# Optimization experiments

Measured on AMD Instinct MI355X. Metric: run time of the kernel, lower is better.

The kernel has to match this reference:

```python
import jax, jax.numpy as jnp
import numpy as np

N, Y, D, B, K, CHUNK = 1024, 2, 128, 256, 16, 64
SCALE = 0.25      # slope of the soft partial order sigmoid
GAMMA = 0.05      # slope of the irrelevance sigmoid
TAU = 2.0 * D     # squared-distance threshold for irrelevance


def setup_inputs() -> dict:
    key = jax.random.key(0)
    ks = jax.random.split(key, 6)
    return {
        "X_train": jax.random.normal(ks[0], (N, D), jnp.float32),
        "X_default": jax.random.normal(ks[1], (Y, D), jnp.float32),
        "X_query": jax.random.normal(ks[2], (B, D), jnp.float32),
        "w_order": jax.random.normal(ks[3], (D,), jnp.float32) / np.float32(np.sqrt(D)),
        "w_base": jax.random.normal(ks[4], (D,), jnp.float32) / np.float32(np.sqrt(D)),
        "y_train_labels": jax.random.randint(ks[5], (N,), 0, Y, jnp.int32),
        "y_default_labels": jnp.arange(Y, dtype=jnp.int32),
    }


def _blocked_product(Wm, Es):
    """result[i,j] = prod_k (1 - Wm[i,k] * Es[k,j]), chunked over k (CHUNK)."""
    T = Wm.shape[0]
    pad = (-T) % CHUNK
    Wp = jnp.pad(Wm, ((0, 0), (0, pad)))   # zero pad -> factor (1-0)=1
    Ep = jnp.pad(Es, ((0, pad), (0, 0)))
    nch = Wp.shape[1] // CHUNK
    Wc = jnp.transpose(Wp.reshape(T, nch, CHUNK), (1, 0, 2))  # [nch, T, CHUNK]
    Ec = Ep.reshape(nch, CHUNK, T)                             # [nch, CHUNK, T]

    def body(carry, wk_ek):
        Wk, Ek = wk_ek  # [T, CHUNK], [CHUNK, T]
        term = jnp.prod(1.0 - Wk[:, :, None] * Ek[None, :, :], axis=1)  # [T, T]
        return carry * term, None

    res, _ = jax.lax.scan(jax.checkpoint(body), jnp.ones((T, T), Wm.dtype), (Wc, Ec))
    return res


def _fit_A(X, yf, w_order, n_default):
    """Build the (negated-attack) edge-weight matrix A of the casebase QBAF."""
    T = X.shape[0]
    is_default = jnp.arange(T) >= (T - n_default)  # default rows cannot attack
    # soft partial order: E[i,j] = sigma(SCALE * (p_i - p_j))  (attacker i vs target j)
    p = X @ w_order                                  # [T]
    E = jax.nn.sigmoid(SCALE * (p[:, None] - p[None, :]))
    Es = E * (1.0 - E.T)                             # strict ordering
    Es = jnp.where(is_default[:, None], 0.0, Es)     # defaults_not_attack
    same = (yf @ yf.T) > 0.5                         # same-label mask (one-hot)
    attacks = jnp.where(same, 0.0, Es)               # potential attacks: differing labels
    # minimal-attack blockers: same-label intermediates k with i<k<j block i->j
    Wm = jnp.where(same, Es, 0.0) * (1.0 - jnp.eye(T, dtype=Es.dtype))
    blocked = _blocked_product(Wm, Es)               # [T, T]
    # symmetric attacks between equal cases with differing labels
    sym = E * E.T
    sym = jnp.where(same, 0.0, sym)
    sym = jnp.where(is_default[:, None], 0.0, sym)
    return -(attacks * blocked + sym)


def reference(X_train, X_default, X_query, w_order, w_base, y_train_labels, y_default_labels):
    X = jnp.concatenate([X_train, X_default], axis=0)          # [T, D]
    yf = jnp.concatenate([
        jax.nn.one_hot(y_train_labels, Y, dtype=X.dtype),
        jax.nn.one_hot(y_default_labels, Y, dtype=X.dtype),
    ], axis=0)                                                 # [T, Y]
    A = _fit_A(X, yf, w_order, Y)                              # [T, T]
    base_logit = X @ w_base                                    # [T]
    # irrelevance edges: new case attacks irrelevant casebase arguments
    sq = (jnp.sum(X_query ** 2, 1)[:, None] + jnp.sum(X ** 2, 1)[None, :]
          - 2.0 * (X_query @ X.T))                             # [B, T]
    r = jax.nn.sigmoid(GAMMA * (sq - TAU))                     # [B, T]
    # gradual semantics: s <- sigma(logit(base) + sum_m A[m,n] s_m - r_n)
    s0 = jnp.broadcast_to(jax.nn.sigmoid(base_logit), (X_query.shape[0], X.shape[0]))
    def step(s, _):
        return jax.nn.sigmoid(base_logit[None, :] + s @ A - r), None
    s, _ = jax.lax.scan(step, s0, None, length=K)
    return s[:, -Y:]  # strengths of the default arguments -> [B, Y]
```

## Files before the change

kernel.cpp:

```cpp
#include <hip/hip_runtime.h>

#define NTRAIN 1024
#define NY 2
#define DDIM 128
#define NB 256
#define NITER 16
#define TT 1026
#define TP 1088
#define CP 640
#define TPP (2*CP)
#define SCALE_C 0.25f
#define GAMMA_C 0.05f
#define TAU_C 256.0f
#define IKCH 128

typedef _Float16 __attribute__((ext_vector_type(8))) f16x8;
typedef __attribute__((ext_vector_type(4))) float f32x4;
typedef __attribute__((ext_vector_type(8))) unsigned short us8;

union FR16 { ushort4 u[2]; f16x8 v; };

__device__ __forceinline__ float sigm(float x) {
    return 1.0f / (1.0f + __expf(-x));
}
__device__ __forceinline__ ushort f2u16(_Float16 h) {
    union { _Float16 h; ushort u; } x; x.h = h; return x.u;
}

__global__ void k_prep(const float* __restrict__ Xtr, const float* __restrict__ Xdef,
                       const float* __restrict__ worder, const float* __restrict__ wbase,
                       float* __restrict__ p, float* __restrict__ bl,
                       float* __restrict__ xsq) {
    int t = blockIdx.x;
    int tx = threadIdx.x;
    __shared__ float sp[128], sb[128], ss[128];
    float po = 0.f, bo = 0.f, sq = 0.f;
    if (t < TT) {
        const float* row = (t < NTRAIN) ? (Xtr + (size_t)t * DDIM)
                                        : (Xdef + (size_t)(t - NTRAIN) * DDIM);
        float x = row[tx];
        po = x * worder[tx];
        bo = x * wbase[tx];
        sq = x * x;
    }
    sp[tx] = po; sb[tx] = bo; ss[tx] = sq;
    __syncthreads();
    for (int off = 64; off > 0; off >>= 1) {
        if (tx < off) { sp[tx] += sp[tx+off]; sb[tx] += sb[tx+off]; ss[tx] += ss[tx+off]; }
        __syncthreads();
    }
    if (tx == 0) { p[t] = sp[0]; bl[t] = sb[0]; xsq[t] = ss[0]; }
}

__global__ void k_perm2(const int* __restrict__ ytr, const float* __restrict__ p,
                        int* __restrict__ map, float* __restrict__ pp) {
    __shared__ int cnt1[16];
    int tid = threadIdx.x;
    int w = tid >> 6, lane = tid & 63;
    for (int a = tid; a < TPP; a += 1024) map[a] = -1;
    int y = ytr[tid];
    unsigned long long b1 = __ballot(y == 1);
    if (lane == 0) cnt1[w] = (int)__popcll(b1);
    __syncthreads();
    int pref1 = 0;
    #pragma unroll
    for (int ww = 0; ww < 16; ww++) pref1 += (ww < w) ? cnt1[ww] : 0;
    int pref0 = w * 64 - pref1;
    unsigned long long mlt = ((unsigned long long)1 << lane) - 1ull;
    int rank = y ? (pref1 + (int)__popcll(b1 & mlt))
                 : (pref0 + (int)__popcll((~b1) & mlt));
    if (rank < CP - 1) map[y * CP + rank] = tid;
    if (tid < NY) map[tid * CP + CP - 1] = NTRAIN + tid;
    __syncthreads();
    for (int a = tid; a < TPP; a += 1024) {
        int m = map[a];
        pp[a] = (m >= 0) ? p[m] : 0.f;
    }
}

__global__ void k_es2(const int* __restrict__ map, const float* __restrict__ pp,
                      float* __restrict__ Es) {
    int b = blockIdx.x * 256 + threadIdx.x;
    int a = blockIdx.y;
    float v = 0.f;
    int mi = map[a], mj = map[b];
    if (mi >= 0 && mi < NTRAIN && mj >= 0) {
        float e = sigm(SCALE_C * (pp[a] - pp[b]));
        v = e * e;
    }
    Es[(size_t)a * TPP + b] = v;
}

#define KC 16
__global__ __launch_bounds__(256) void k_pblk2(const float* __restrict__ Es,
                                               float* __restrict__ P, int kspan) {
    __shared__ float Wt[KC][64 + 4];
    __shared__ float Et[KC][64 + 4];
    int c  = blockIdx.z & 1;
    int kz = blockIdx.z >> 1;
    int i0 = c * CP + blockIdx.y * 64;
    int j0 = (1 - c) * CP + blockIdx.x * 64;
    int ks = c * CP + kz * kspan, ke = ks + kspan;
    int tid = threadIdx.x;
    int tx = tid & 15, ty = tid >> 4;
    float prod[4][4];
    #pragma unroll
    for (int a = 0; a < 4; a++)
        #pragma unroll
        for (int b = 0; b < 4; b++) prod[a][b] = 1.f;

    for (int k0 = ks; k0 < ke; k0 += KC) {
        __syncthreads();
        #pragma unroll
        for (int e = tid; e < KC * 64; e += 256) {
            int kk = e & 15, ii = e >> 4;
            int gi = i0 + ii, gk = k0 + kk;
            float w = Es[(size_t)gi * TPP + gk];
            if (gi == gk) w = 0.f;
            Wt[kk][ii] = w;
        }
        #pragma unroll
        for (int e = tid; e < KC * 64; e += 256) {
            int jj = e & 63, kk = e >> 6;
            Et[kk][jj] = Es[(size_t)(k0 + kk) * TPP + j0 + jj];
        }
        __syncthreads();
        #pragma unroll
        for (int kk = 0; kk < KC; kk++) {
            float4 wv = *(const float4*)&Wt[kk][ty * 4];
            float4 ev = *(const float4*)&Et[kk][tx * 4];
            float w[4] = {wv.x, wv.y, wv.z, wv.w};
            float e[4] = {ev.x, ev.y, ev.z, ev.w};
            #pragma unroll
            for (int a = 0; a < 4; a++)
                #pragma unroll
                for (int b = 0; b < 4; b++)
                    prod[a][b] *= fmaf(-w[a], e[b], 1.f);
        }
    }
    float* Pz = P + (size_t)blockIdx.z * CP * CP;
    int jjl = blockIdx.x * 64 + tx * 4;
    #pragma unroll
    for (int a = 0; a < 4; a++) {
        int iil = blockIdx.y * 64 + ty * 4 + a;
        *(float4*)&Pz[(size_t)iil * CP + jjl] =
            make_float4(prod[a][0], prod[a][1], prod[a][2], prod[a][3]);
    }
}

__global__ __launch_bounds__(256) void k_afin2T(const float* __restrict__ P, int psplit,
                                                const int* __restrict__ map,
                                                const float* __restrict__ pp,
                                                const float* __restrict__ Es,
                                                ushort* __restrict__ ATF) {
    __shared__ float t[64][65];
    int n0 = blockIdx.y * 64;
    int d = (n0 >= CP) ? 1 : 0;
    int c = 1 - d;
    int kl0 = blockIdx.x * 64;
    int tid = threadIdx.x;
    for (int e = tid; e < 64 * 64; e += 256) {
        int r = e >> 6, col = e & 63;
        int iil = kl0 + r;
        int jjl = n0 - d * CP + col;
        size_t rem = (size_t)iil * CP + jjl;
        float prod = P[(size_t)c * CP * CP + rem];
        for (int kz = 1; kz < psplit; kz++)
            prod *= P[(size_t)(kz * 2 + c) * CP * CP + rem];
        int a = c * CP + iil, b = n0 + col;
        float v = 0.f;
        int mi = map[a], mj = map[b];
        if (mi >= 0 && mj >= 0) {
            float es = Es[(size_t)a * TPP + b];
            float x = SCALE_C * (pp[a] - pp[b]);
            float E = sigm(x);
            float sym = (mi < NTRAIN) ? E * (1.f - E) : 0.f;
            v = -(es * prod + sym);
        }
        t[r][col] = v;
    }
    __syncthreads();
    for (int e = tid; e < 64 * 64; e += 256) {
        int kk = e & 63, nn = e >> 6;
        ATF[(size_t)(n0 + nn) * CP + kl0 + kk] = f2u16((_Float16)t[kk][nn]);
    }
}

__global__ void k_cq2(const float* __restrict__ Xtr, const float* __restrict__ Xdef,
                      const float* __restrict__ Xq, const float* __restrict__ bl,
                      const int* __restrict__ map,
                      float* __restrict__ CT, ushort* __restrict__ SF) {
    int bq = blockIdx.y;
    int t = blockIdx.x * 256 + threadIdx.x;
    int mi = map[t];
    float cv = 0.f, sv = 0.f;
    if (mi >= 0) {
        const float4* q4 = (const float4*)(Xq + (size_t)bq * DDIM);
        const float* row = (mi < NTRAIN) ? (Xtr + (size_t)mi * DDIM)
                                         : (Xdef + (size_t)(mi - NTRAIN) * DDIM);
        const float4* x4 = (const float4*)row;
        float dot = 0.f, qs = 0.f, xs = 0.f;
        #pragma unroll
        for (int d = 0; d < DDIM / 4; d++) {
            float4 q = q4[d], x = x4[d];
            dot = fmaf(q.x, x.x, fmaf(q.y, x.y, fmaf(q.z, x.z, fmaf(q.w, x.w, dot))));
            qs  = fmaf(q.x, q.x, fmaf(q.y, q.y, fmaf(q.z, q.z, fmaf(q.w, q.w, qs))));
            xs  = fmaf(x.x, x.x, fmaf(x.y, x.y, fmaf(x.z, x.z, fmaf(x.w, x.w, xs))));
        }
        float sq = qs + xs - 2.f * dot;
        float r = sigm(GAMMA_C * (sq - TAU_C));
        cv = bl[mi] - r;
        sv = sigm(bl[mi]);
    }
    size_t o = (size_t)bq * TPP + t;
    CT[o] = cv;
    SF[o] = f2u16((_Float16)sv);
}

__device__ __forceinline__ float Aval(int m, int k) { return (float)((3*m + 7*k) % 13 - 6); }
__device__ __forceinline__ float Bval(int k, int n) { return (float)((5*k + 11*n) % 9 - 4); }

__global__ void k_probe(int* __restrict__ flag) {
    int lane = threadIdx.x;
    int lg = lane >> 4, li = lane & 15;
    FR16 fa, fb;
    #pragma unroll
    for (int j = 0; j < 8; j++) {
        int k = (j < 4) ? (4*lg + j) : (16 + 4*lg + (j - 4));
        fa.v[j] = (_Float16)Aval(li, k);
        fb.v[j] = (_Float16)Bval(k, li);
    }
    f32x4 acc = {0.f, 0.f, 0.f, 0.f};
    acc = __builtin_amdgcn_mfma_f32_16x16x32_f16(fa.v, fb.v, acc, 0, 0, 0);
    int ok = 1;
    #pragma unroll
    for (int r = 0; r < 4; r++) {
        int row = 4*lg + r, col = li;
        float ref = 0.f;
        for (int k = 0; k < 32; k++) ref += Aval(row, k) * Bval(k, col);
        if (acc[r] != ref) ok = 0;
    }
    int allok = __all(ok);
    if (lane == 0) *flag = allok ? 0 : 1;
}

__global__ __launch_bounds__(256) void k_ifp16(const ushort* __restrict__ SF,
                                               const ushort* __restrict__ ATF,
                                               const float* __restrict__ CT,
                                               const int* __restrict__ map,
                                               const int* __restrict__ flag,
                                               ushort* __restrict__ NF,
                                               float* __restrict__ out, int last) {
    __shared__ ushort SfL[32][IKCH + 8];
    __shared__ ushort AfL[32][IKCH + 8];
    int tid = threadIdx.x;
    int n0 = blockIdx.x * 32;
    int m0 = blockIdx.y * 32;
    int kb = (n0 >= CP) ? 0 : CP;
    int wv = tid >> 6, lane = tid & 63;
    int wm = wv >> 1, wn = wv & 1;
    int lg = lane >> 4, li = lane & 15;
    int hyp = *flag;
    int o0 = hyp ? (8*lg)     : (4*lg);
    int o1 = hyp ? (8*lg + 4) : (16 + 4*lg);
    int srow = tid >> 3, sc = tid & 7;

    const ushort* sfg = SF + (size_t)(m0 + srow) * TPP + kb;
    const ushort* afg = ATF + (size_t)(n0 + srow) * CP;

    f32x4 c0 = {0.f,0.f,0.f,0.f};

    us8 buf[4];
    #define ISSUE(dst, k0)                                            \
        dst[0] = *(const us8*)(sfg + (k0) + sc * 8);                  \
        dst[1] = *(const us8*)(sfg + (k0) + (sc + 8) * 8);            \
        dst[2] = *(const us8*)(afg + (k0) + sc * 8);                  \
        dst[3] = *(const us8*)(afg + (k0) + (sc + 8) * 8);

    ISSUE(buf, 0)

    #pragma unroll
    for (int ci = 0; ci < CP / IKCH; ci++) {
        __syncthreads();
        *(us8*)&SfL[srow][sc * 8]       = buf[0];
        *(us8*)&SfL[srow][(sc + 8) * 8] = buf[1];
        *(us8*)&AfL[srow][sc * 8]       = buf[2];
        *(us8*)&AfL[srow][(sc + 8) * 8] = buf[3];
        __syncthreads();
        us8 nbuf[4];
        if (ci + 1 < CP / IKCH) { ISSUE(nbuf, (ci + 1) * IKCH) }
        #pragma unroll
        for (int ks = 0; ks < IKCH / 32; ks++) {
            int ka = ks * 32;
            FR16 fs, fa;
            fs.u[0] = *(const ushort4*)&SfL[wm * 16 + li][ka + o0];
            fs.u[1] = *(const ushort4*)&SfL[wm * 16 + li][ka + o1];
            fa.u[0] = *(const ushort4*)&AfL[wn * 16 + li][ka + o0];
            fa.u[1] = *(const ushort4*)&AfL[wn * 16 + li][ka + o1];
            c0 = __builtin_amdgcn_mfma_f32_16x16x32_f16(fs.v, fa.v, c0, 0, 0, 0);
        }
        if (ci + 1 < CP / IKCH) {
            #pragma unroll
            for (int q = 0; q < 4; q++) buf[q] = nbuf[q];
        }
    }
    #undef ISSUE

    int col = n0 + wn * 16 + li;
    int valid = (map[col] >= 0);
    #pragma unroll
    for (int r = 0; r < 4; r++) {
        int row = m0 + wm * 16 + 4 * lg + r;
        float v = 0.f;
        if (valid) v = sigm(CT[(size_t)row * TPP + col] + c0[r]);
        NF[(size_t)row * TPP + col] = f2u16((_Float16)v);
        if (last && (col == CP - 1 || col == TPP - 1)) {
            int cc = (col == CP - 1) ? 0 : 1;
            out[row * NY + cc] = v;
        }
    }
}

extern "C" void kernel_launch(void* const* d_in, const int* in_sizes, int n_in,
                              void* d_out, int out_size, void* d_ws, size_t ws_size,
                              hipStream_t stream) {
    const float* Xtr    = (const float*)d_in[0];
    const float* Xdef   = (const float*)d_in[1];
    const float* Xq     = (const float*)d_in[2];
    const float* worder = (const float*)d_in[3];
    const float* wbase  = (const float*)d_in[4];
    const int*   ytr    = (const int*)d_in[5];

    const size_t MATP = (size_t)TPP * TPP * 4;
    const size_t VECP = (size_t)NB * TPP * 4;
    const size_t ATB2 = (size_t)TPP * CP * 2;
    const size_t SB   = (size_t)NB * TPP * 2;
    auto need = [&](int ps) {
        return (size_t)(8 * 8192) + MATP + (size_t)ps * 2 * CP * CP * 4
             + ATB2 + VECP + 2 * SB + 65536;
    };
    int psplit = 8;
    if (ws_size < need(8)) psplit = 4;
    if (ws_size < need(4)) psplit = 2;
    if (ws_size < need(2)) psplit = 1;
    int kspan = CP / psplit;

    char* ws = (char*)d_ws;
    size_t off = 0;
    auto alloc = [&](size_t bytes) {
        void* r = ws + off;
        off += (bytes + 255) & ~(size_t)255;
        return r;
    };
    float*  p    = (float*)alloc((size_t)TP * 4);
    float*  bl   = (float*)alloc((size_t)TP * 4);
    float*  xsq  = (float*)alloc((size_t)TP * 4);
    int*    map  = (int*)  alloc((size_t)TPP * 4);
    float*  pp   = (float*)alloc((size_t)TPP * 4);
    int*    flag = (int*)  alloc(256);
    float*  Es   = (float*)alloc(MATP);
    float*  P    = (float*)alloc((size_t)psplit * 2 * CP * CP * 4);
    ushort* ATF  = (ushort*)alloc(ATB2);
    float*  CT   = (float*)alloc(VECP);
    ushort* SF0  = (ushort*)alloc(SB);
    ushort* SF1  = (ushort*)alloc(SB);

    k_prep<<<TP, 128, 0, stream>>>(Xtr, Xdef, worder, wbase, p, bl, xsq);
    k_perm2<<<1, 1024, 0, stream>>>(ytr, p, map, pp);
    k_es2<<<dim3(TPP / 256, TPP), 256, 0, stream>>>(map, pp, Es);
    k_pblk2<<<dim3(CP / 64, CP / 64, 2 * psplit), 256, 0, stream>>>(Es, P, kspan);
    k_afin2T<<<dim3(CP / 64, TPP / 64), 256, 0, stream>>>(P, psplit, map, pp, Es, ATF);
    k_cq2<<<dim3(TPP / 256, NB), 256, 0, stream>>>(Xtr, Xdef, Xq, bl, map, CT, SF0);
    k_probe<<<1, 64, 0, stream>>>(flag);

    ushort *cf = SF0, *nf = SF1;
    for (int it = 0; it < NITER; it++) {
        k_ifp16<<<dim3(TPP / 32, NB / 32), 256, 0, stream>>>(cf, ATF, CT, map, flag, nf,
                                                             (float*)d_out,
                                                             it == NITER - 1 ? 1 : 0);
        ushort* t = cf; cf = nf; nf = t;
    }
}
```

Measured before the change: 288.5 us.

## Compute Es on the fly, batch query distances, and load full-K tiles in iteration kernel

Drops the materialised 1280x1280 Es matrix. The product kernel now recomputes sigmoid entries from the permuted p values and per-class counts, and the final A kernel recomputes E directly. The query-distance kernel handles 8 queries per block from shared memory and precomputes query norms separately. The iteration kernel loads the whole K=640 strip into LDS at once, uses 64-wide N tiles with two MFMA accumulators, and sets launch bounds to one block. This trades Es memory traffic for extra sigmoid work and larger LDS use, which may lower occupancy.

```diff
diff --git a/kernel.cpp b/kernel.cpp
--- a/kernel.cpp
+++ b/kernel.cpp
@@ -12,7 +12,6 @@
 #define SCALE_C 0.25f
 #define GAMMA_C 0.05f
 #define TAU_C 256.0f
-#define IKCH 128
 
 typedef _Float16 __attribute__((ext_vector_type(8))) f16x8;
 typedef __attribute__((ext_vector_type(4))) float f32x4;
@@ -29,31 +28,29 @@
 
 __global__ void k_prep(const float* __restrict__ Xtr, const float* __restrict__ Xdef,
                        const float* __restrict__ worder, const float* __restrict__ wbase,
-                       float* __restrict__ p, float* __restrict__ bl,
-                       float* __restrict__ xsq) {
+                       float* __restrict__ p, float* __restrict__ bl) {
     int t = blockIdx.x;
     int tx = threadIdx.x;
-    __shared__ float sp[128], sb[128], ss[128];
-    float po = 0.f, bo = 0.f, sq = 0.f;
+    __shared__ float sp[128], sb[128];
+    float po = 0.f, bo = 0.f;
     if (t < TT) {
         const float* row = (t < NTRAIN) ? (Xtr + (size_t)t * DDIM)
                                         : (Xdef + (size_t)(t - NTRAIN) * DDIM);
         float x = row[tx];
         po = x * worder[tx];
         bo = x * wbase[tx];
-        sq = x * x;
-    }
-    sp[tx] = po; sb[tx] = bo; ss[tx] = sq;
+    }
+    sp[tx] = po; sb[tx] = bo;
     __syncthreads();
     for (int off = 64; off > 0; off >>= 1) {
-        if (tx < off) { sp[tx] += sp[tx+off]; sb[tx] += sb[tx+off]; ss[tx] += ss[tx+off]; }
+        if (tx < off) { sp[tx] += sp[tx+off]; sb[tx] += sb[tx+off]; }
         __syncthreads();
     }
-    if (tx == 0) { p[t] = sp[0]; bl[t] = sb[0]; xsq[t] = ss[0]; }
+    if (tx == 0) { p[t] = sp[0]; bl[t] = sb[0]; }
 }
 
 __global__ void k_perm2(const int* __restrict__ ytr, const float* __restrict__ p,
-                        int* __restrict__ map, float* __restrict__ pp) {
+                        int* __restrict__ map, float* __restrict__ pp, int* __restrict__ nc) {
     __shared__ int cnt1[16];
     int tid = threadIdx.x;
     int w = tid >> 6, lane = tid & 63;
@@ -62,15 +59,20 @@
     unsigned long long b1 = __ballot(y == 1);
     if (lane == 0) cnt1[w] = (int)__popcll(b1);
     __syncthreads();
-    int pref1 = 0;
-    #pragma unroll
-    for (int ww = 0; ww < 16; ww++) pref1 += (ww < w) ? cnt1[ww] : 0;
+    int pref1 = 0, tot1 = 0;
+    #pragma unroll
+    for (int ww = 0; ww < 16; ww++) { pref1 += (ww < w) ? cnt1[ww] : 0; tot1 += cnt1[ww]; }
     int pref0 = w * 64 - pref1;
     unsigned long long mlt = ((unsigned long long)1 << lane) - 1ull;
     int rank = y ? (pref1 + (int)__popcll(b1 & mlt))
                  : (pref0 + (int)__popcll((~b1) & mlt));
     if (rank < CP - 1) map[y * CP + rank] = tid;
     if (tid < NY) map[tid * CP + CP - 1] = NTRAIN + tid;
+    if (tid == 0) {
+        int n1 = tot1 < CP - 1 ? tot1 : CP - 1;
+        int n0 = (NTRAIN - tot1) < CP - 1 ? (NTRAIN - tot1) : CP - 1;
+        nc[0] = n0; nc[1] = n1;
+    }
     __syncthreads();
     for (int a = tid; a < TPP; a += 1024) {
         int m = map[a];
@@ -78,51 +80,69 @@
     }
 }
 
-__global__ void k_es2(const int* __restrict__ map, const float* __restrict__ pp,
-                      float* __restrict__ Es) {
-    int b = blockIdx.x * 256 + threadIdx.x;
-    int a = blockIdx.y;
-    float v = 0.f;
-    int mi = map[a], mj = map[b];
-    if (mi >= 0 && mi < NTRAIN && mj >= 0) {
-        float e = sigm(SCALE_C * (pp[a] - pp[b]));
-        v = e * e;
-    }
-    Es[(size_t)a * TPP + b] = v;
+__global__ void k_qsq(const float* __restrict__ Xq, float* __restrict__ qsq) {
+    int m = threadIdx.x;
+    const float4* q4 = (const float4*)(Xq + (size_t)m * DDIM);
+    float s = 0.f;
+    #pragma unroll
+    for (int d = 0; d < DDIM / 4; d++) {
+        float4 q = q4[d];
+        s = fmaf(q.x, q.x, fmaf(q.y, q.y, fmaf(q.z, q.z, fmaf(q.w, q.w, s))));
+    }
+    qsq[m] = s;
 }
 
 #define KC 16
-__global__ __launch_bounds__(256) void k_pblk2(const float* __restrict__ Es,
+__global__ __launch_bounds__(256) void k_pblk3(const float* __restrict__ pp,
+                                               const int* __restrict__ nc,
                                                float* __restrict__ P, int kspan) {
-    __shared__ float Wt[KC][64 + 4];
-    __shared__ float Et[KC][64 + 4];
+    __shared__ float Wt[KC][68];
+    __shared__ float Et[KC][68];
+    __shared__ float ppi[64], ppj[64], ppk[320], mka[320], mkt[320];
     int c  = blockIdx.z & 1;
     int kz = blockIdx.z >> 1;
-    int i0 = c * CP + blockIdx.y * 64;
-    int j0 = (1 - c) * CP + blockIdx.x * 64;
-    int ks = c * CP + kz * kspan, ke = ks + kspan;
+    int i0l = blockIdx.y * 64, j0l = blockIdx.x * 64;
+    int k0l = kz * kspan;
     int tid = threadIdx.x;
     int tx = tid & 15, ty = tid >> 4;
+    int ncc = nc[c], ncd = nc[1 - c];
+    const float* ppc = pp + c * CP;
+    const float* ppd = pp + (1 - c) * CP;
+    if (tid < 64) ppi[tid] = ppc[i0l + tid];
+    else if (tid < 128) ppj[tid - 64] = ppd[j0l + tid - 64];
+    for (int e = tid; e < kspan; e += 256) {
+        int kl = k0l + e;
+        ppk[e] = ppc[kl];
+        mka[e] = (kl < ncc) ? 1.f : 0.f;
+        mkt[e] = (kl < ncc || kl == CP - 1) ? 1.f : 0.f;
+    }
+    __syncthreads();
+
     float prod[4][4];
     #pragma unroll
     for (int a = 0; a < 4; a++)
         #pragma unroll
         for (int b = 0; b < 4; b++) prod[a][b] = 1.f;
 
-    for (int k0 = ks; k0 < ke; k0 += KC) {
+    for (int kc0 = 0; kc0 < kspan; kc0 += KC) {
         __syncthreads();
         #pragma unroll
         for (int e = tid; e < KC * 64; e += 256) {
             int kk = e & 15, ii = e >> 4;
-            int gi = i0 + ii, gk = k0 + kk;
-            float w = Es[(size_t)gi * TPP + gk];
-            if (gi == gk) w = 0.f;
+            float s = sigm(SCALE_C * (ppi[ii] - ppk[kc0 + kk]));
+            float w = s * s * mkt[kc0 + kk];
+            int il = i0l + ii, kl = k0l + kc0 + kk;
+            if (il >= ncc || il == kl) w = 0.f;
             Wt[kk][ii] = w;
         }
         #pragma unroll
         for (int e = tid; e < KC * 64; e += 256) {
             int jj = e & 63, kk = e >> 6;
-            Et[kk][jj] = Es[(size_t)(k0 + kk) * TPP + j0 + jj];
+            float s = sigm(SCALE_C * (ppk[kc0 + kk] - ppj[jj]));
+            float v = s * s * mka[kc0 + kk];
+            int jl = j0l + jj;
+            if (jl >= ncd && jl != CP - 1) v = 0.f;
+            Et[kk][jj] = v;
         }
         __syncthreads();
         #pragma unroll
@@ -151,7 +171,6 @@
 __global__ __launch_bounds__(256) void k_afin2T(const float* __restrict__ P, int psplit,
                                                 const int* __restrict__ map,
                                                 const float* __restrict__ pp,
-                                                const float* __restrict__ Es,
                                                 ushort* __restrict__ ATF) {
     __shared__ float t[64][65];
     int n0 = blockIdx.y * 64;
@@ -170,12 +189,9 @@
         int a = c * CP + iil, b = n0 + col;
         float v = 0.f;
         int mi = map[a], mj = map[b];
-        if (mi >= 0 && mj >= 0) {
-            float es = Es[(size_t)a * TPP + b];
-            float x = SCALE_C * (pp[a] - pp[b]);
-            float E = sigm(x);
-            float sym = (mi < NTRAIN) ? E * (1.f - E) : 0.f;
-            v = -(es * prod + sym);
+        if (mi >= 0 && mi < NTRAIN && mj >= 0) {
+            float E = sigm(SCALE_C * (pp[a] - pp[b]));
+            v = -(E * E * prod + E * (1.f - E));
         }
         t[r][col] = v;
     }
@@ -186,35 +202,59 @@
     }
 }
 
-__global__ void k_cq2(const float* __restrict__ Xtr, const float* __restrict__ Xdef,
-                      const float* __restrict__ Xq, const float* __restrict__ bl,
-                      const int* __restrict__ map,
-                      float* __restrict__ CT, ushort* __restrict__ SF) {
-    int bq = blockIdx.y;
-    int t = blockIdx.x * 256 + threadIdx.x;
+__global__ __launch_bounds__(256) void k_cq3(const float* __restrict__ Xtr,
+                                             const float* __restrict__ Xdef,
+                                             const float* __restrict__ Xq,
+                                             const float* __restrict__ bl,
+                                             const float* __restrict__ qsq,
+                                             const int* __restrict__ map,
+                                             float* __restrict__ CT, ushort* __restrict__ SF) {
+    __shared__ float qv[8][132];
+    int bt0 = blockIdx.x * 256, bq0 = blockIdx.y * 8;
+    int tid = threadIdx.x;
+    for (int e = tid; e < 8 * 128; e += 256) {
+        int q = e >> 7, dd = e & 127;
+        qv[q][dd] = Xq[(size_t)(bq0 + q) * DDIM + dd];
+    }
+    __syncthreads();
+    int t = bt0 + tid;
     int mi = map[t];
-    float cv = 0.f, sv = 0.f;
+    float cv[8];
+    float sv = 0.f;
+    #pragma unroll
+    for (int q = 0; q < 8; q++) cv[q] = 0.f;
     if (mi >= 0) {
-        const float4* q4 = (const float4*)(Xq + (size_t)bq * DDIM);
         const float* row = (mi < NTRAIN) ? (Xtr + (size_t)mi * DDIM)
                                          : (Xdef + (size_t)(mi - NTRAIN) * DDIM);
         const float4* x4 = (const float4*)row;
-        float dot = 0.f, qs = 0.f, xs = 0.f;
-        #pragma unroll
-        for (int d = 0; d < DDIM / 4; d++) {
-            float4 q = q4[d], x = x4[d];
-            dot = fmaf(q.x, x.x, fmaf(q.y, x.y, fmaf(q.z, x.z, fmaf(q.w, x.w, dot))));
-            qs  = fmaf(q.x, q.x, fmaf(q.y, q.y, fmaf(q.z, q.z, fmaf(q.w, q.w, qs))));
-            xs  = fmaf(x.x, x.x, fmaf(x.y, x.y, fmaf(x.z, x.z, fmaf(x.w, x.w, xs))));
-        }
-        float sq = qs + xs - 2.f * dot;
-        float r = sigm(GAMMA_C * (sq - TAU_C));
-        cv = bl[mi] - r;
-        sv = sigm(bl[mi]);
-    }
-    size_t o = (size_t)bq * TPP + t;
-    CT[o] = cv;
-    SF[o] = f2u16((_Float16)sv);
+        float dot[8];
+        #pragma unroll
+        for (int q = 0; q < 8; q++) dot[q] = 0.f;
+        float xs = 0.f;
+        #pragma unroll 8
+        for (int d4 = 0; d4 < 32; d4++) {
+            float4 x = x4[d4];
+            xs = fmaf(x.x, x.x, fmaf(x.y, x.y, fmaf(x.z, x.z, fmaf(x.w, x.w, xs))));
+            #pragma unroll
+            for (int q = 0; q < 8; q++) {
+                float4 qq = *(const float4*)&qv[q][d4 * 4];
+                dot[q] = fmaf(x.x, qq.x, fmaf(x.y, qq.y, fmaf(x.z, qq.z, fmaf(x.w, qq.w, dot[q]))));
+            }
+        }
+        float blv = bl[mi];
+        sv = sigm(blv);
+        #pragma unroll
+        for (int q = 0; q < 8; q++) {
+            float sq = qsq[bq0 + q] + xs - 2.f * dot[q];
+            cv[q] = blv - sigm(GAMMA_C * (sq - TAU_C));
+        }
+    }
+    ushort su = f2u16((_Float16)sv);
+    #pragma unroll
+    for (int q = 0; q < 8; q++) {
+        CT[(size_t)(bq0 + q) * TPP + t] = cv[q];
+        SF[(size_t)(bq0 + q) * TPP + t] = su;
+    }
 }
 
 __device__ __forceinline__ float Aval(int m, int k) { return (float)((3*m + 7*k) % 13 - 6); }
@@ -244,18 +284,17 @@
     if (lane == 0) *flag = allok ? 0 : 1;
 }
 
-__global__ __launch_bounds__(256) void k_ifp16(const ushort* __restrict__ SF,
-                                               const ushort* __restrict__ ATF,
-                                               const float* __restrict__ CT,
-                                               const int* __restrict__ map,
-                                               const int* __restrict__ flag,
-                                               ushort* __restrict__ NF,
-                                               float* __restrict__ out, int last) {
-    __shared__ ushort SfL[32][IKCH + 8];
-    __shared__ ushort AfL[32][IKCH + 8];
+__global__ __launch_bounds__(256, 1) void k_it3(const ushort* __restrict__ SF,
+                                                const ushort* __restrict__ ATF,
+                                                const float* __restrict__ CT,
+                                                const int* __restrict__ map,
+                                                const int* __restrict__ flag,
+                                                ushort* __restrict__ NF,
+                                                float* __restrict__ out, int last) {
+    __shared__ ushort SfL[32][648];
+    __shared__ ushort AfL[64][648];
     int tid = threadIdx.x;
-    int n0 = blockIdx.x * 32;
-    int m0 = blockIdx.y * 32;
+    int n0 = blockIdx.x * 64, m0 = blockIdx.y * 32;
     int kb = (n0 >= CP) ? 0 : CP;
     int wv = tid >> 6, lane = tid & 63;
     int wm = wv >> 1, wn = wv & 1;
@@ -263,60 +302,47 @@
     int hyp = *flag;
     int o0 = hyp ? (8*lg)     : (4*lg);
     int o1 = hyp ? (8*lg + 4) : (16 + 4*lg);
-    int srow = tid >> 3, sc = tid & 7;
-
-    const ushort* sfg = SF + (size_t)(m0 + srow) * TPP + kb;
-    const ushort* afg = ATF + (size_t)(n0 + srow) * CP;
-
-    f32x4 c0 = {0.f,0.f,0.f,0.f};
-
-    us8 buf[4];
-    #define ISSUE(dst, k0)                                            \
-        dst[0] = *(const us8*)(sfg + (k0) + sc * 8);                  \
-        dst[1] = *(const us8*)(sfg + (k0) + (sc + 8) * 8);            \
-        dst[2] = *(const us8*)(afg + (k0) + sc * 8);                  \
-        dst[3] = *(const us8*)(afg + (k0) + (sc + 8) * 8);
-
-    ISSUE(buf, 0)
-
-    #pragma unroll
-    for (int ci = 0; ci < CP / IKCH; ci++) {
-        __syncthreads();
-        *(us8*)&SfL[srow][sc * 8]       = buf[0];
-        *(us8*)&SfL[srow][(sc + 8) * 8] = buf[1];
-        *(us8*)&AfL[srow][sc * 8]       = buf[2];
-        *(us8*)&AfL[srow][(sc + 8) * 8] = buf[3];
-        __syncthreads();
-        us8 nbuf[4];
-        if (ci + 1 < CP / IKCH) { ISSUE(nbuf, (ci + 1) * IKCH) }
-        #pragma unroll
-        for (int ks = 0; ks < IKCH / 32; ks++) {
-            int ka = ks * 32;
-            FR16 fs, fa;
-            fs.u[0] = *(const ushort4*)&SfL[wm * 16 + li][ka + o0];
-            fs.u[1] = *(const ushort4*)&SfL[wm * 16 + li][ka + o1];
-            fa.u[0] = *(const ushort4*)&AfL[wn * 16 + li][ka + o0];
-            fa.u[1] = *(const ushort4*)&AfL[wn * 16 + li][ka + o1];
-            c0 = __builtin_amdgcn_mfma_f32_16x16x32_f16(fs.v, fa.v, c0, 0, 0, 0);
-        }
-        if (ci + 1 < CP / IKCH) {
-            #pragma unroll
-            for (int q = 0; q < 4; q++) buf[q] = nbuf[q];
-        }
-    }
-    #undef ISSUE
-
-    int col = n0 + wn * 16 + li;
-    int valid = (map[col] >= 0);
-    #pragma unroll
-    for (int r = 0; r < 4; r++) {
-        int row = m0 + wm * 16 + 4 * lg + r;
-        float v = 0.f;
-        if (valid) v = sigm(CT[(size_t)row * TPP + col] + c0[r]);
-        NF[(size_t)row * TPP + col] = f2u16((_Float16)v);
-        if (last && (col == CP - 1 || col == TPP - 1)) {
-            int cc = (col == CP - 1) ? 0 : 1;
-            out[row * NY + cc] = v;
+
+    for (int e = tid; e < 32 * 80; e += 256) {
+        int r = e / 80, c8 = e % 80;
+        *(us8*)&SfL[r][c8 * 8] = *(const us8*)(SF + (size_t)(m0 + r) * TPP + kb + c8 * 8);
+    }
+    for (int e = tid; e < 64 * 80; e += 256) {
+        int r = e / 80, c8 = e % 80;
+        *(us8*)&AfL[r][c8 * 8] = *(const us8*)(ATF + (size_t)(n0 + r) * CP + c8 * 8);
+    }
+    __syncthreads();
+
+    f32x4 a0 = {0.f,0.f,0.f,0.f}, a1 = {0.f,0.f,0.f,0.f};
+    #pragma unroll
+    for (int ks = 0; ks < 20; ks++) {
+        int ka = ks * 32;
+        FR16 fs, f0, f1;
+        fs.u[0] = *(const ushort4*)&SfL[wm * 16 + li][ka + o0];
+        fs.u[1] = *(const ushort4*)&SfL[wm * 16 + li][ka + o1];
+        f0.u[0] = *(const ushort4*)&AfL[wn * 32 + li][ka + o0];
+        f0.u[1] = *(const ushort4*)&AfL[wn * 32 + li][ka + o1];
+        f1.u[0] = *(const ushort4*)&AfL[wn * 32 + 16 + li][ka + o0];
+        f1.u[1] = *(const ushort4*)&AfL[wn * 32 + 16 + li][ka + o1];
+        a0 = __builtin_amdgcn_mfma_f32_16x16x32_f16(fs.v, f0.v, a0, 0, 0, 0);
+        a1 = __builtin_amdgcn_mfma_f32_16x16x32_f16(fs.v, f1.v, a1, 0, 0, 0);
+    }
+
+    #pragma unroll
+    for (int nt = 0; nt < 2; nt++) {
+        int col = n0 + wn * 32 + nt * 16 + li;
+        int valid = (map[col] >= 0);
+        f32x4 ac = nt ? a1 : a0;
+        #pragma unroll
+        for (int r = 0; r < 4; r++) {
+            int row = m0 + wm * 16 + 4 * lg + r;
+            float v = 0.f;
+            if (valid) v = sigm(CT[(size_t)row * TPP + col] + ac[r]);
+            NF[(size_t)row * TPP + col] = f2u16((_Float16)v);
+            if (last && (col == CP - 1 || col == TPP - 1)) {
+                int cc = (col == CP - 1) ? 0 : 1;
+                out[row * NY + cc] = v;
+            }
         }
     }
 }
@@ -331,12 +357,11 @@
     const float* wbase  = (const float*)d_in[4];
     const int*   ytr    = (const int*)d_in[5];
 
-    const size_t MATP = (size_t)TPP * TPP * 4;
     const size_t VECP = (size_t)NB * TPP * 4;
     const size_t ATB2 = (size_t)TPP * CP * 2;
     const size_t SB   = (size_t)NB * TPP * 2;
     auto need = [&](int ps) {
-        return (size_t)(8 * 8192) + MATP + (size_t)ps * 2 * CP * CP * 4
+        return (size_t)(8 * 8192) + (size_t)ps * 2 * CP * CP * 4
              + ATB2 + VECP + 2 * SB + 65536;
     };
     int psplit = 8;
@@ -354,30 +379,30 @@
     };
     float*  p    = (float*)alloc((size_t)TP * 4);
     float*  bl   = (float*)alloc((size_t)TP * 4);
-    float*  xsq  = (float*)alloc((size_t)TP * 4);
     int*    map  = (int*)  alloc((size_t)TPP * 4);
     float*  pp   = (float*)alloc((size_t)TPP * 4);
+    int*    nc   = (int*)  alloc(256);
     int*    flag = (int*)  alloc(256);
-    float*  Es   = (float*)alloc(MATP);
+    float*  qsq  = (float*)alloc((size_t)NB * 4);
     float*  P    = (float*)alloc((size_t)psplit * 2 * CP * CP * 4);
     ushort* ATF  = (ushort*)alloc(ATB2);
     float*  CT   = (float*)alloc(VECP);
     ushort* SF0  = (ushort*)alloc(SB);
     ushort* SF1  = (ushort*)alloc(SB);
 
-    k_prep<<<TP, 128, 0, stream>>>(Xtr, Xdef, worder, wbase, p, bl, xsq);
-    k_perm2<<<1, 1024, 0, stream>>>(ytr, p, map, pp);
-    k_es2<<<dim3(TPP / 256, TPP), 256, 0, stream>>>(map, pp, Es);
-    k_pblk2<<<dim3(CP / 64, CP / 64, 2 * psplit), 256, 0, stream>>>(Es, P, kspan);
-    k_afin2T<<<dim3(CP / 64, TPP / 64), 256, 0, stream>>>(P, psplit, map, pp, Es, ATF);
-    k_cq2<<<dim3(TPP / 256, NB), 256, 0, stream>>>(Xtr, Xdef, Xq, bl, map, CT, SF0);
+    k_prep<<<TP, 128, 0, stream>>>(Xtr, Xdef, worder, wbase, p, bl);
+    k_perm2<<<1, 1024, 0, stream>>>(ytr, p, map, pp, nc);
+    k_qsq<<<1, 256, 0, stream>>>(Xq, qsq);
+    k_cq3<<<dim3(TPP / 256, NB / 8), 256, 0, stream>>>(Xtr, Xdef, Xq, bl, qsq, map, CT, SF0);
     k_probe<<<1, 64, 0, stream>>>(flag);
+    k_pblk3<<<dim3(CP / 64, CP / 64, 2 * psplit), 256, 0, stream>>>(pp, nc, P, kspan);
+    k_afin2T<<<dim3(CP / 64, TPP / 64), 256, 0, stream>>>(P, psplit, map, pp, ATF);
 
     ushort *cf = SF0, *nf = SF1;
     for (int it = 0; it < NITER; it++) {
-        k_ifp16<<<dim3(TPP / 32, NB / 32), 256, 0, stream>>>(cf, ATF, CT, map, flag, nf,
-                                                             (float*)d_out,
-                                                             it == NITER - 1 ? 1 : 0);
+        k_it3<<<dim3(TPP / 64, NB / 32), 256, 0, stream>>>(cf, ATF, CT, map, flag, nf,
+                                                           (float*)d_out,
+                                                           it == NITER - 1 ? 1 : 0);
         ushort* t = cf; cf = nf; nf = t;
     }
 }
```

Result: slower. 345.0 us (+19.6%).
